# Optimization experiments

Measured on AMD Instinct MI355X. Metric: run time of the kernel, lower is better.

## Reference

```python
import jax, jax.numpy as jnp
from jax import lax
import numpy as np
import math

B = 2; H = 64; W = 64; HW = H * W
CIN = 128; CH = 64          # in_chans, in_chans//2
E = 192; DEPTH = 2          # embed_dim, depth
DIN = 384; DST = 4; DTR = 12; KC = 4   # d_inner, d_state, dt_rank, d_conv
NC = 9
SAMPLE = HW // 2            # round(h*w*self_ratio), self_ratio=0.5
LE = HW - SAMPLE            # number of mask==0 (easy) tokens per row


def setup_inputs() -> dict:
    key = jax.random.key(0)
    ks = jax.random.split(key, 16)
    rn = lambda k, s, sc: jax.random.normal(k, s, jnp.float32) * sc
    return {
        'x': rn(ks[0], (B, CIN, H, W), 1.0),
        'head_id': 0,
        'sp_w': rn(ks[1], (1, CH, 1, 1), 1.0 / math.sqrt(CH)),
        'sp_b': jnp.zeros((1,), jnp.float32),
        'c0_w': rn(ks[2], (E, CIN, 1, 1), 1.0 / math.sqrt(CIN)),
        'c0_b': jnp.zeros((E,), jnp.float32),
        'blk_norm_w': jnp.ones((DEPTH, E), jnp.float32),
        'blk_conv_w': rn(ks[3], (DEPTH, E, E, 3, 3), 1.0 / math.sqrt(9 * E)),
        'blk_conv_b': jnp.zeros((DEPTH, E), jnp.float32),
        'm_in_w': rn(ks[4], (DEPTH, 2 * DIN, E), 1.0 / math.sqrt(E)),
        'm_conv_w': rn(ks[5], (DEPTH, DIN, KC), 1.0 / math.sqrt(KC)),
        'm_conv_b': jnp.zeros((DEPTH, DIN), jnp.float32),
        'm_x_w': rn(ks[6], (DEPTH, DTR + 2 * DST, DIN), 1.0 / math.sqrt(DIN)),
        'm_dt_w': rn(ks[7], (DEPTH, DIN, DTR), 1.0 / math.sqrt(DTR)),
        'm_dt_b': rn(ks[8], (DEPTH, DIN), 0.1),
        'm_Alog': jnp.tile(jnp.log(jnp.arange(1, DST + 1, dtype=jnp.float32)), (DEPTH, DIN, 1)),
        'm_D': jnp.ones((DEPTH, DIN), jnp.float32),
        'm_out_w': rn(ks[9], (DEPTH, E, DIN), 1.0 / math.sqrt(DIN)),
        'ln_w': jnp.ones((E,), jnp.float32),
        'ln_b': jnp.zeros((E,), jnp.float32),
        'h_conv_w': rn(ks[10], (E, E, 3, 3), 1.0 / math.sqrt(9 * E)),
        'h_bn_w': jnp.ones((E,), jnp.float32),
        'h_bn_b': jnp.zeros((E,), jnp.float32),
        'h_cls_w': rn(ks[11], (NC, E, 1, 1), 1.0 / math.sqrt(E)),
        'h_cls_b': jnp.zeros((NC,), jnp.float32),
    }


def conv2d(x, w, b=None, pad=0, dil=1):
    y = lax.conv_general_dilated(x, w, (1, 1), [(pad, pad), (pad, pad)],
                                 rhs_dilation=(dil, dil),
                                 dimension_numbers=('NCHW', 'OIHW', 'NCHW'))
    return y if b is None else y + b[None, :, None, None]


def silu(x):
    return x * jax.nn.sigmoid(x)


def mamba_mixer(xe, in_w, conv_w, conv_b, x_w, dt_w, dt_b, Alog, Dp, out_w):
    # xe: [B, L, E] easy tokens; standard Mamba selective scan (d_state=4, d_conv=4)
    Bn, L, _ = xe.shape
    xz = jnp.einsum('ble,de->bld', xe, in_w)          # [B,L,2*DIN]
    xh, z = jnp.split(xz, 2, axis=-1)
    xp = jnp.pad(xh, ((0, 0), (KC - 1, 0), (0, 0)))   # causal depthwise conv
    xc = conv_b + sum(conv_w[:, k] * xp[:, k:k + L, :] for k in range(KC))
    xc = silu(xc)
    dbl = jnp.einsum('bld,rd->blr', xc, x_w)
    dt, Bm, Cm = dbl[..., :DTR], dbl[..., DTR:DTR + DST], dbl[..., DTR + DST:]
    dt = jax.nn.softplus(jnp.einsum('blr,dr->bld', dt, dt_w) + dt_b)
    A = -jnp.exp(Alog)                                 # [DIN, DST]
    dA = jnp.exp(dt[..., None] * A)                    # [B,L,DIN,DST]
    dBx = dt[..., None] * Bm[:, :, None, :] * xc[..., None]

    def step(h, inp):
        dA_t, dBx_t, C_t = inp
        h = dA_t * h + dBx_t
        return h, jnp.einsum('bdn,bn->bd', h, C_t)

    h0 = jnp.zeros((Bn, DIN, DST), xe.dtype)
    _, ys = lax.scan(step, h0, (jnp.moveaxis(dA, 1, 0), jnp.moveaxis(dBx, 1, 0), jnp.moveaxis(Cm, 1, 0)))
    y = jnp.moveaxis(ys, 0, 1) + Dp * xc
    y = y * silu(z)
    return jnp.einsum('bld,ed->ble', y, out_w)


def snm_forward(x, sp_w, sp_b, c0_w, c0_b, blk_norm_w, blk_conv_w, blk_conv_b,
                m_in_w, m_conv_w, m_conv_b, m_x_w, m_dt_w, m_dt_b, m_Alog, m_D, m_out_w,
                ln_w, ln_b, h_conv_w, h_bn_w, h_bn_b, h_cls_w, h_cls_b):
    res, imgf = jnp.split(x, 2, axis=1)
    res = res * res                                    # prepocess_residual('square')
    simple_pred = jax.nn.sigmoid(conv2d(res, sp_w, sp_b))
    scores = (simple_pred + res.mean(1, keepdims=True)).reshape(B, HW)
    idx = jnp.argsort(scores, axis=1)[:, :SAMPLE]      # topk smallest
    feats = imgf.transpose(0, 2, 3, 1).reshape(B, HW, CH)

    def per_batch(f_i, idx_i):
        bank = f_i[idx_i]                              # [SAMPLE, CH]
        d2 = (jnp.sum(f_i * f_i, -1, keepdims=True)
              + jnp.sum(bank * bank, -1)[None, :]
              - 2.0 * f_i @ bank.T)
        d = jnp.sqrt(jnp.maximum(d2, 0.0))
        d = d.at[idx_i, jnp.arange(SAMPLE)].set(jnp.inf)   # exclude self matches
        nns = jnp.argmin(lax.stop_gradient(d), axis=1)
        return bank[nns] - f_i

    sres = jax.vmap(per_batch)(feats, idx)
    sres = sres.reshape(B, H, W, CH).transpose(0, 3, 1, 2)
    sres = sres * sres                                 # prepocess_residual('square')
    x2 = jnp.concatenate([res, sres], axis=1)          # [B, CIN, H, W]

    mask = jnp.zeros((B, HW), jnp.float32).at[jnp.arange(B)[:, None], idx].set(1.0)
    easy_idx = jnp.argsort(mask, axis=1)[:, :LE]       # stable: mask==0 positions in order
    bidx = jnp.arange(B)[:, None]

    fea = conv2d(x2, c0_w, c0_b)                       # [B,E,H,W]
    hidden = fea.reshape(B, E, HW).transpose(0, 2, 1)  # [B,L,E]
    residual = None
    for d in range(DEPTH):
        residual = hidden if residual is None else hidden + residual
        hid = residual * lax.rsqrt(jnp.mean(residual * residual, -1, keepdims=True) + 1e-5) * blk_norm_w[d]
        him = hid.transpose(0, 2, 1).reshape(B, E, H, W)
        him = conv2d(him, blk_conv_w[d], blk_conv_b[d], pad=1)
        hid = him.reshape(B, E, HW).transpose(0, 2, 1)
        easy = hid[bidx, easy_idx]                     # gather mask==0 tokens
        mixed = mamba_mixer(easy, m_in_w[d], m_conv_w[d], m_conv_b[d], m_x_w[d],
                            m_dt_w[d], m_dt_b[d], m_Alog[d], m_D[d], m_out_w[d])
        hidden = hid.at[bidx, easy_idx].set(mixed)     # scatter back

    out = hidden + residual
    mu = out.mean(-1, keepdims=True)
    var = jnp.mean((out - mu) ** 2, -1, keepdims=True)
    out = (out - mu) * lax.rsqrt(var + 1e-5) * ln_w + ln_b
    f = out.transpose(0, 2, 1).reshape(B, E, H, W)

    # head (atrous_rate=3): dilated conv (no bias) + BN(eval, running stats 0/1) + ReLU + 1x1
    h1 = conv2d(f, h_conv_w, pad=3, dil=3)
    bn_scale = h_bn_w / jnp.sqrt(1.0 + 1e-5)
    h1 = jax.nn.relu(h1 * bn_scale[None, :, None, None] + h_bn_b[None, :, None, None])
    logits = conv2d(h1, h_cls_w, h_cls_b)
    return simple_pred, logits


def reference(x, head_id, sp_w, sp_b, c0_w, c0_b, blk_norm_w, blk_conv_w, blk_conv_b,
              m_in_w, m_conv_w, m_conv_b, m_x_w, m_dt_w, m_dt_b, m_Alog, m_D, m_out_w,
              ln_w, ln_b, h_conv_w, h_bn_w, h_bn_b, h_cls_w, h_cls_b):
    # head_id=0 selects branch 0; only branch-0 params are materialized.
    return snm_forward(x, sp_w, sp_b, c0_w, c0_b, blk_norm_w, blk_conv_w, blk_conv_b,
                       m_in_w, m_conv_w, m_conv_b, m_x_w, m_dt_w, m_dt_b, m_Alog, m_D, m_out_w,
                       ln_w, ln_b, h_conv_w, h_bn_w, h_bn_b, h_cls_w, h_cls_b)
```

## Files before the change

### kernel.cpp

```cpp
#include <hip/hip_runtime.h>
#include <hip/hip_bf16.h>
#include <math.h>

#define BB 2
#define HWp 4096
#define CH 64
#define CIN 128
#define EE 192
#define DIN 384
#define DST 4
#define DTR 12
#define KC 4
#define NCc 9
#define SAMPLE 2048
#define LEc 2048
#define NCH 128
#define CLEN 16
#define NSPLIT 8
#define PADW 70
#define PADP 3

typedef __attribute__((ext_vector_type(8))) short bf16x8;
typedef __attribute__((ext_vector_type(4))) float f32x4;

__device__ __forceinline__ float sigmoid_fast(float x){ return 1.0f/(1.0f+__expf(-x)); }
__device__ __forceinline__ float softplus_f(float x){ return fmaxf(x,0.0f) + log1pf(expf(-fabsf(x))); }

__device__ __forceinline__ void split_bf16(float v, unsigned short& h, unsigned short& l){
  __hip_bfloat16 bh = __float2bfloat16(v);
  h = *(unsigned short*)&bh;
  float r = v - __bfloat162float(bh);
  __hip_bfloat16 bl = __float2bfloat16(r);
  l = *(unsigned short*)&bl;
}

#define SZ_WTBLK_BF (2*9*EE*EE)
#define SZ_WTHEAD_BF (9*EE*EE)
#define SZ_WTIN (2*EE*2*DIN)
#define SZ_WTOUT (2*DIN*EE)
#define SZ_WTC0 (CIN*EE)
#define SZ_WT_TOTAL (SZ_WTBLK_BF+SZ_WTHEAD_BF+SZ_WTIN+SZ_WTOUT+SZ_WTC0)

__global__ void prep_weights(const float* blk_w, const float* head_w, const float* in_w,
                             const float* out_w, const float* c0_w,
                             __hip_bfloat16* wtb_blk, __hip_bfloat16* wtb_head,
                             float* wt_in, float* wt_out, float* wt_c0){
  int i = blockIdx.x*256 + threadIdx.x;
  if (i >= SZ_WT_TOTAL) return;
  int o = i;
  if (o < SZ_WTBLK_BF){
    int j = o & 7;
    int lane = (o>>3) & 63;
    int nt = (o/512) % 3;
    int e = (o/1536) % 6;
    int tap = (o/9216) % 9;
    int eoB = (o/82944) % 4;
    int d = o / 331776;
    int m = lane & 15, kg = lane >> 4;
    int eo = eoB*48 + nt*16 + m;
    int ei = e*32 + kg*8 + j;
    wtb_blk[o] = __float2bfloat16(blk_w[(((d*EE+eo)*EE+ei)*9)+tap]);
    return;
  }
  o -= SZ_WTBLK_BF;
  if (o < SZ_WTHEAD_BF){
    int j = o & 7;
    int lane = (o>>3) & 63;
    int nt = (o/512) % 3;
    int e = (o/1536) % 6;
    int tap = (o/9216) % 9;
    int eoB = (o/82944) % 4;
    int m = lane & 15, kg = lane >> 4;
    int eo = eoB*48 + nt*16 + m;
    int ei = e*32 + kg*8 + j;
    wtb_head[o] = __float2bfloat16(head_w[((eo*EE+ei)*9)+tap]);
    return;
  }
  o -= SZ_WTHEAD_BF;
  if (o < SZ_WTIN){
    int dd = o % (2*DIN); int e = (o/(2*DIN))%EE; int d = o/(2*DIN*EE);
    wt_in[o] = in_w[((d*2*DIN)+dd)*EE + e]; return;
  }
  o -= SZ_WTIN;
  if (o < SZ_WTOUT){
    int eo = o%EE; int dch=(o/EE)%DIN; int d = o/(EE*DIN);
    wt_out[o] = out_w[((d*EE+eo)*DIN)+dch]; return;
  }
  o -= SZ_WTOUT;
  { int e = o%EE; int c = o/EE;  wt_c0[o] = c0_w[e*CIN + c]; }
}

__global__ __launch_bounds__(256) void k_prep2(const float* __restrict__ x, const float* sp_w,
                       const float* sp_b, float* __restrict__ res2, float* __restrict__ feats,
                       float* scores, float* outSP){
  __shared__ float tile[CIN][33];
  int t = threadIdx.x;
  int p0 = blockIdx.x * 32;
  int b = p0 >> 12; int prow = p0 & 4095;
  const float* xb = x + (size_t)b*CIN*HWp + prow;
  #pragma unroll
  for (int i=0;i<4;i++){
    int idx = i*256 + t;
    int c = idx >> 3;
    int p4 = idx & 7;
    float4 v = *(const float4*)(xb + (size_t)c*HWp + p4*4);
    tile[c][p4*4+0]=v.x; tile[c][p4*4+1]=v.y; tile[c][p4*4+2]=v.z; tile[c][p4*4+3]=v.w;
  }
  __syncthreads();
  int lane = t & 63;
  int wv = t >> 6;
  float sw = sp_w[lane];
  float sb = sp_b[0];
  #pragma unroll
  for (int k=0;k<8;k++){
    int p = wv*8 + k;
    float v = tile[lane][p];
    float r2 = v*v;
    float f = tile[64+lane][p];
    int g = p0 + p;
    res2[(size_t)g*CH + lane] = r2;
    feats[(size_t)g*CH + lane] = f;
    float aS = r2*sw, aM = r2;
    #pragma unroll
    for (int msk=32; msk>0; msk>>=1){
      aS += __shfl_xor(aS, msk, 64);
      aM += __shfl_xor(aM, msk, 64);
    }
    if (lane == 0){
      float sp = 1.0f/(1.0f+expf(-(aS + sb)));
      outSP[g] = sp;
      scores[g] = sp + aM*(1.0f/CH);
    }
  }
}

__global__ void k_zero(int* p, int n){
  int g = blockIdx.x*256+threadIdx.x;
  if (g < n) p[g] = 0;
}

__global__ void k_rank2(const float* scores, int* ranks){
  int b = blockIdx.z;
  int t = threadIdx.x;
  int p = blockIdx.x*256 + t;
  int j0 = blockIdx.y*256;
  __shared__ float s[256];
  s[t] = scores[b*HWp + j0 + t];
  float sp = scores[b*HWp + p];
  __syncthreads();
  int r = 0;
  #pragma unroll 8
  for (int jj=0;jj<256;jj++){
    float sj = s[jj];
    int j = j0 + jj;
    r += (sj < sp || (sj == sp && j < p)) ? 1 : 0;
  }
  atomicAdd(&ranks[b*HWp+p], r);
}

__global__ __launch_bounds__(1024) void k_easy(const int* ranks, int* idx_sorted, int* easy_idx){
  int b = blockIdx.x; int t = threadIdx.x;
  __shared__ int buf[1024];
  int i0 = t*4;
  int r0 = ranks[b*HWp+i0];
  int r1 = ranks[b*HWp+i0+1];
  int r2 = ranks[b*HWp+i0+2];
  int r3 = ranks[b*HWp+i0+3];
  int f0 = r0 >= SAMPLE, f1 = r1 >= SAMPLE, f2 = r2 >= SAMPLE, f3 = r3 >= SAMPLE;
  if (!f0) idx_sorted[b*SAMPLE + r0] = i0;
  if (!f1) idx_sorted[b*SAMPLE + r1] = i0+1;
  if (!f2) idx_sorted[b*SAMPLE + r2] = i0+2;
  if (!f3) idx_sorted[b*SAMPLE + r3] = i0+3;
  int cnt = f0+f1+f2+f3;
  buf[t] = cnt;
  __syncthreads();
  for (int off=1; off<1024; off<<=1){
    int v = buf[t];
    int a = (t>=off) ? buf[t-off] : 0;
    __syncthreads();
    buf[t] = v + a;
    __syncthreads();
  }
  int pre = buf[t] - cnt;
  int base = b*LEc;
  if (f0) easy_idx[base+pre++] = i0;
  if (f1) easy_idx[base+pre++] = i0+1;
  if (f2) easy_idx[base+pre++] = i0+2;
  if (f3) easy_idx[base+pre]   = i0+3;
}

__global__ void k_split(const float* __restrict__ feats, unsigned short* __restrict__ fhi,
                        unsigned short* __restrict__ flo){
  int g = blockIdx.x*256 + threadIdx.x;
  float4 v = ((const float4*)feats)[g];
  ushort4 h, l;
  split_bf16(v.x, h.x, l.x);
  split_bf16(v.y, h.y, l.y);
  split_bf16(v.z, h.z, l.z);
  split_bf16(v.w, h.w, l.w);
  ((ushort4*)fhi)[g] = h;
  ((ushort4*)flo)[g] = l;
}

__global__ __launch_bounds__(64) void k_bank(const float* __restrict__ feats, const int* __restrict__ idx_sorted,
                       float* __restrict__ bnorm, unsigned short* __restrict__ bankhi,
                       unsigned short* __restrict__ banklo){
  int t = blockIdx.x*64+threadIdx.x;
  int b = t>>11;
  int row = idx_sorted[t];
  const float4* fr = (const float4*)(feats + (size_t)(b*HWp + row)*CH);
  ushort4* oh = (ushort4*)(bankhi + (size_t)t*CH);
  ushort4* ol = (ushort4*)(banklo + (size_t)t*CH);
  float s=0;
  #pragma unroll
  for (int k=0;k<16;k++){
    float4 v = fr[k];
    s += v.x*v.x+v.y*v.y+v.z*v.z+v.w*v.w;
    ushort4 h, l;
    split_bf16(v.x, h.x, l.x);
    split_bf16(v.y, h.y, l.y);
    split_bf16(v.z, h.z, l.z);
    split_bf16(v.w, h.w, l.w);
    oh[k] = h; ol[k] = l;
  }
  bnorm[t] = s;
}

__global__ __launch_bounds__(256) void k_nn_mfma(const unsigned short* __restrict__ fhi,
        const unsigned short* __restrict__ flo, const unsigned short* __restrict__ bankhi,
        const unsigned short* __restrict__ banklo, const float* __restrict__ bnorm,
        const int* __restrict__ idx_sorted, float* __restrict__ pval, int* __restrict__ pidx){
  int lane = threadIdx.x & 63;
  int wv = threadIdx.x >> 6;
  int m = lane & 15, kg = lane >> 4;
  int b = blockIdx.z;
  int qrel0 = blockIdx.x*64 + wv*16;
  int jsplit = blockIdx.y;
  const short* qh = (const short*)fhi + ((size_t)(b*HWp + qrel0 + m))*CH + kg*8;
  const short* ql = (const short*)flo + ((size_t)(b*HWp + qrel0 + m))*CH + kg*8;
  bf16x8 Ah0 = *(const bf16x8*)(qh);
  bf16x8 Ah1 = *(const bf16x8*)(qh + 32);
  bf16x8 Al0 = *(const bf16x8*)(ql);
  bf16x8 Al1 = *(const bf16x8*)(ql + 32);
  float best0=1e30f,best1=1e30f,best2=1e30f,best3=1e30f;
  int bj0=0,bj1=0,bj2=0,bj3=0;
  for (int jt=0; jt<16; jt++){
    int jb = jsplit*256 + jt*16;
    int j = jb + m;
    const short* bh = (const short*)bankhi + ((size_t)(b*SAMPLE + j))*CH + kg*8;
    const short* bl = (const short*)banklo + ((size_t)(b*SAMPLE + j))*CH + kg*8;
    bf16x8 Bh0 = *(const bf16x8*)(bh);
    bf16x8 Bh1 = *(const bf16x8*)(bh + 32);
    bf16x8 Bl0 = *(const bf16x8*)(bl);
    bf16x8 Bl1 = *(const bf16x8*)(bl + 32);
    f32x4 acc = {0,0,0,0};
    acc = __builtin_amdgcn_mfma_f32_16x16x32_bf16(Ah0, Bh0, acc, 0,0,0);
    acc = __builtin_amdgcn_mfma_f32_16x16x32_bf16(Ah1, Bh1, acc, 0,0,0);
    acc = __builtin_amdgcn_mfma_f32_16x16x32_bf16(Al0, Bh0, acc, 0,0,0);
    acc = __builtin_amdgcn_mfma_f32_16x16x32_bf16(Al1, Bh1, acc, 0,0,0);
    acc = __builtin_amdgcn_mfma_f32_16x16x32_bf16(Ah0, Bl0, acc, 0,0,0);
    acc = __builtin_amdgcn_mfma_f32_16x16x32_bf16(Ah1, Bl1, acc, 0,0,0);
    acc = __builtin_amdgcn_mfma_f32_16x16x32_bf16(Al0, Bl0, acc, 0,0,0);
    acc = __builtin_amdgcn_mfma_f32_16x16x32_bf16(Al1, Bl1, acc, 0,0,0);
    float bn = bnorm[b*SAMPLE + j];
    int src = idx_sorted[b*SAMPLE + j];
    float v0 = bn - 2.0f*acc[0];
    float v1 = bn - 2.0f*acc[1];
    float v2 = bn - 2.0f*acc[2];
    float v3 = bn - 2.0f*acc[3];
    int qp = qrel0 + kg*4;
    if (src != qp   && v0 < best0){ best0 = v0; bj0 = j; }
    if (src != qp+1 && v1 < best1){ best1 = v1; bj1 = j; }
    if (src != qp+2 && v2 < best2){ best2 = v2; bj2 = j; }
    if (src != qp+3 && v3 < best3){ best3 = v3; bj3 = j; }
  }
  #pragma unroll
  for (int mask=1; mask<16; mask<<=1){
    float ov; int oj;
    ov = __shfl_xor(best0, mask, 64); oj = __shfl_xor(bj0, mask, 64);
    if (ov < best0 || (ov == best0 && oj < bj0)){ best0 = ov; bj0 = oj; }
    ov = __shfl_xor(best1, mask, 64); oj = __shfl_xor(bj1, mask, 64);
    if (ov < best1 || (ov == best1 && oj < bj1)){ best1 = ov; bj1 = oj; }
    ov = __shfl_xor(best2, mask, 64); oj = __shfl_xor(bj2, mask, 64);
    if (ov < best2 || (ov == best2 && oj < bj2)){ best2 = ov; bj2 = oj; }
    ov = __shfl_xor(best3, mask, 64); oj = __shfl_xor(bj3, mask, 64);
    if (ov < best3 || (ov == best3 && oj < bj3)){ best3 = ov; bj3 = oj; }
  }
  if (m == 0){
    int qg = b*HWp + qrel0 + kg*4;
    pval[(qg+0)*NSPLIT + jsplit] = best0; pidx[(qg+0)*NSPLIT + jsplit] = bj0;
    pval[(qg+1)*NSPLIT + jsplit] = best1; pidx[(qg+1)*NSPLIT + jsplit] = bj1;
    pval[(qg+2)*NSPLIT + jsplit] = best2; pidx[(qg+2)*NSPLIT + jsplit] = bj2;
    pval[(qg+3)*NSPLIT + jsplit] = best3; pidx[(qg+3)*NSPLIT + jsplit] = bj3;
  }
}

__global__ __launch_bounds__(64) void k_nn_resolve(const float* feats, const int* idx_sorted,
                             const float* pval, const int* pidx, float* sres2){
  int q = blockIdx.x*64+threadIdx.x;
  int b = q>>12;
  float best = 1e30f; int bj = 0;
  for (int s=0;s<NSPLIT;s++){
    float v = pval[q*NSPLIT+s]; int j = pidx[q*NSPLIT+s];
    if (v < best){ best = v; bj = j; }
  }
  int row = idx_sorted[b*SAMPLE + bj];
  const float4* fr = (const float4*)(feats + (size_t)q*CH);
  const float4* br = (const float4*)(feats + (size_t)(b*HWp+row)*CH);
  float4* out = (float4*)(sres2 + (size_t)q*CH);
  #pragma unroll
  for (int k=0;k<16;k++){
    float4 a = br[k], c = fr[k];
    float4 r;
    r.x=a.x-c.x; r.y=a.y-c.y; r.z=a.z-c.z; r.w=a.w-c.w;
    r.x*=r.x; r.y*=r.y; r.z*=r.z; r.w*=r.w;
    out[k] = r;
  }
}

__global__ __launch_bounds__(192) void k_c0(const float* res2, const float* sres2, const float* wt_c0,
                                            const float* c0_b, float* hidden){
  __shared__ float xin[CIN][20];
  int base = blockIdx.x * 16;
  int t = threadIdx.x;
  for (int i=t; i<16*CIN; i+=192){
    int px = i >> 7, c = i & 127;
    float v = (c < CH) ? res2[(base+px)*CH + c] : sres2[(base+px)*CH + (c-CH)];
    xin[c][px] = v;
  }
  __syncthreads();
  int e = t;
  float bias = c0_b[e];
  float acc[16];
  #pragma unroll
  for (int px=0;px<16;px++) acc[px]=bias;
  for (int c=0;c<CIN;c++){
    float w = wt_c0[c*EE + e];
    const float4* vr = (const float4*)(&xin[c][0]);
    float4 v0=vr[0], v1=vr[1], v2=vr[2], v3=vr[3];
    acc[0]+=v0.x*w; acc[1]+=v0.y*w; acc[2]+=v0.z*w; acc[3]+=v0.w*w;
    acc[4]+=v1.x*w; acc[5]+=v1.y*w; acc[6]+=v1.z*w; acc[7]+=v1.w*w;
    acc[8]+=v2.x*w; acc[9]+=v2.y*w; acc[10]+=v2.z*w; acc[11]+=v2.w*w;
    acc[12]+=v3.x*w; acc[13]+=v3.y*w; acc[14]+=v3.z*w; acc[15]+=v3.w*w;
  }
  #pragma unroll
  for (int px=0;px<16;px++) hidden[(base+px)*EE + e] = acc[px];
}

__global__ __launch_bounds__(192) void k_rms(const float* hidden, float* residual,
                                             __hip_bfloat16* __restrict__ xpad,
                                             const float* norm_w, int first){
  int row = blockIdx.x; int e = threadIdx.x;
  int o = row*EE + e;
  float h = hidden[o];
  float r = first ? h : (h + residual[o]);
  residual[o] = r;
  float s = r*r;
  #pragma unroll
  for (int m=32;m>0;m>>=1) s += __shfl_xor(s, m, 64);
  __shared__ float red[3];
  if ((e&63)==0) red[e>>6] = s;
  __syncthreads();
  float tot = red[0]+red[1]+red[2];
  float rms = rsqrtf(tot*(1.0f/EE) + 1e-5f);
  int b = row >> 12; int p = row & 4095; int y = p >> 6; int x = p & 63;
  xpad[((size_t)(b*PADW + y + PADP)*PADW + (x + PADP))*EE + e] = __float2bfloat16(r*rms*norm_w[e]);
}

template<int DIL, int FUSE>
__global__ __launch_bounds__(256,3) void k_conv3s(const __hip_bfloat16* __restrict__ xp,
        const __hip_bfloat16* __restrict__ wt, const float* __restrict__ bias,
        const float* __restrict__ bnw, const float* __restrict__ bnb,
        float* __restrict__ out){
  __shared__ short wlds[2][9216];
  int t = threadIdx.x;
  int lane = t & 63;
  int wv = t >> 6;
  int m = lane & 15, kg = lane >> 4;
  int rb = blockIdx.x;
  int b = rb >> 6, y = rb & 63;
  int eoB = blockIdx.y;
  int x = wv*16 + m;
  const short* xs = (const short*)xp;
  const short* ws = (const short*)wt + (size_t)eoB * 82944;
  int aBase0 = ((b*PADW + y + PADP)*PADW + (x + PADP))*EE + kg*8;

  f32x4 acc0={0,0,0,0}, acc1={0,0,0,0}, acc2={0,0,0,0};

  {
    const ushort4* src = (const ushort4*)(ws);
    ushort4* dst = (ushort4*)(&wlds[0][0]);
    #pragma unroll
    for (int k=0;k<9;k++) dst[k*256+t] = src[k*256+t];
  }
  bf16x8 curA[6];
  {
    int aB = aBase0 + ((-1)*DIL*PADW + (-1)*DIL)*EE;
    #pragma unroll
    for (int e=0;e<6;e++) curA[e] = *(const bf16x8*)(xs + aB + e*32);
  }
  __syncthreads();

  for (int tap=0; tap<9; tap++){
    int cur = tap & 1;
    ushort4 nxtW[9];
    bf16x8 nxtA[6];
    if (tap < 8){
      const ushort4* src = (const ushort4*)(ws + (size_t)(tap+1)*9216);
      #pragma unroll
      for (int k=0;k<9;k++) nxtW[k] = src[k*256+t];
      int ky = (tap+1)/3, kx = (tap+1)%3;
      int aB = aBase0 + ((ky-1)*DIL*PADW + (kx-1)*DIL)*EE;
      #pragma unroll
      for (int e=0;e<6;e++) nxtA[e] = *(const bf16x8*)(xs + aB + e*32);
    }
    const short* bl = &wlds[cur][0];
    #pragma unroll
    for (int e=0;e<6;e++){
      bf16x8 b0 = *(const bf16x8*)(bl + (e*3+0)*512 + lane*8);
      bf16x8 b1 = *(const bf16x8*)(bl + (e*3+1)*512 + lane*8);
      bf16x8 b2 = *(const bf16x8*)(bl + (e*3+2)*512 + lane*8);
      acc0 = __builtin_amdgcn_mfma_f32_16x16x32_bf16(curA[e], b0, acc0, 0,0,0);
      acc1 = __builtin_amdgcn_mfma_f32_16x16x32_bf16(curA[e], b1, acc1, 0,0,0);
      acc2 = __builtin_amdgcn_mfma_f32_16x16x32_bf16(curA[e], b2, acc2, 0,0,0);
    }
    if (tap < 8){
      ushort4* dst = (ushort4*)(&wlds[cur^1][0]);
      #pragma unroll
      for (int k=0;k<9;k++) dst[k*256+t] = nxtW[k];
      #pragma unroll
      for (int e=0;e<6;e++) curA[e] = nxtA[e];
    }
    __syncthreads();
  }

  int px0 = y*64 + wv*16 + kg*4;
  #pragma unroll
  for (int nt=0; nt<3; nt++){
    f32x4 a = (nt==0)?acc0:((nt==1)?acc1:acc2);
    int eo = eoB*48 + nt*16 + m;
    float add=0.0f, scale=0.0f, sh=0.0f;
    if (FUSE){ scale = bnw[eo]*rsqrtf(1.0f+1e-5f); sh = bnb[eo]; }
    else add = bias[eo];
    #pragma unroll
    for (int r=0;r<4;r++){
      float v = a[r];
      if (FUSE) v = fmaxf(v*scale + sh, 0.0f);
      else v += add;
      out[((size_t)(b*HWp) + px0 + r)*EE + eo] = v;
    }
  }
}

__global__ __launch_bounds__(256) void k_inproj(const float* hid2, const int* easy_idx, const float* wt_in_d,
                                                float* xh, float* zb){
  __shared__ float sh[EE][12];
  int bid = blockIdx.x;
  int b = bid >> 8; int l0 = (bid & 255)*8;
  int t = threadIdx.x;
  for (int i=t; i<8*EE; i+=256){
    int l = i/EE; int e = i - l*EE;
    int row = easy_idx[b*LEc + l0 + l];
    sh[e][l] = hid2[(b*HWp + row)*EE + e];
  }
  __syncthreads();
  float acc0[8], acc1[8], acc2[8];
  #pragma unroll
  for (int l=0;l<8;l++){ acc0[l]=0; acc1[l]=0; acc2[l]=0; }
  for (int e=0;e<EE;e++){
    float w0 = wt_in_d[e*768 + t];
    float w1 = wt_in_d[e*768 + t + 256];
    float w2 = wt_in_d[e*768 + t + 512];
    const float4* vr = (const float4*)(&sh[e][0]);
    float4 a = vr[0], c = vr[1];
    float v[8] = {a.x,a.y,a.z,a.w,c.x,c.y,c.z,c.w};
    #pragma unroll
    for (int l=0;l<8;l++){ acc0[l]+=v[l]*w0; acc1[l]+=v[l]*w1; acc2[l]+=v[l]*w2; }
  }
  #pragma unroll
  for (int k=0;k<3;k++){
    int dd = t + k*256;
    #pragma unroll
    for (int l=0;l<8;l++){
      float o = (k==0)?acc0[l]:((k==1)?acc1[l]:acc2[l]);
      int rb = b*LEc + l0 + l;
      if (dd < DIN) xh[rb*DIN + dd] = o;
      else zb[rb*DIN + dd - DIN] = o;
    }
  }
}

__global__ __launch_bounds__(128) void k_mpre(const float* xh, const float* cw, const float* cb,
                                              const float* xw, const float* dtw, const float* dtb_w,
                                              float* xc, float* bc, float* dtb){
  int row = blockIdx.x;
  int l = row & 2047;
  int t = threadIdx.x;
  __shared__ float sxc[DIN];
  __shared__ float sdbl[20];
  for (int i=t; i<DIN; i+=128){
    const float* w = cw + i*KC;
    float s = cb[i];
    #pragma unroll
    for (int k=0;k<KC;k++){
      int ls = l - 3 + k;
      if (ls >= 0) s += w[k]*xh[(row-3+k)*DIN + i];
    }
    s = s * sigmoid_fast(s);
    sxc[i] = s;
    xc[row*DIN+i] = s;
  }
  __syncthreads();
  if (t < 20){
    const float* w = xw + t*DIN;
    float a=0,b2=0,c=0,d2=0;
    for (int i=0;i<DIN;i+=4){ a+=sxc[i]*w[i]; b2+=sxc[i+1]*w[i+1]; c+=sxc[i+2]*w[i+2]; d2+=sxc[i+3]*w[i+3]; }
    float o = a+b2+c+d2;
    sdbl[t] = o;
    if (t >= DTR) bc[row*8 + (t-DTR)] = o;
  }
  __syncthreads();
  for (int i=t; i<DIN; i+=128){
    const float* w = dtw + i*DTR;
    float s = dtb_w[i];
    #pragma unroll
    for (int k=0;k<DTR;k++) s += sdbl[k]*w[k];
    dtb[row*DIN+i] = softplus_f(s);
  }
}

__global__ void k_scanA(const float* dt, const float* xc, const float* bc, const float* Alog, float* chnk){
  int g = blockIdx.x*256+threadIdx.x;
  int dch = g % DIN; int c = (g/DIN) % NCH; int b = g/(DIN*NCH);
  float A[4], P[4]={1,1,1,1}, h[4]={0,0,0,0};
  #pragma unroll
  for (int n=0;n<4;n++) A[n] = -__expf(Alog[dch*DST+n]);
  int lbase = b*LEc + c*CLEN;
  for (int s=0;s<CLEN;s++){
    int base = lbase + s;
    float dtv = dt[base*DIN + dch];
    float xcv = xc[base*DIN + dch];
    float dx = dtv*xcv;
    #pragma unroll
    for (int n=0;n<4;n++){
      float dA = __expf(dtv*A[n]);
      float Bn = bc[base*8 + n];
      h[n] = dA*h[n] + dx*Bn;
      P[n] *= dA;
    }
  }
  float* o = chnk + (size_t)g*8;
  #pragma unroll
  for (int n=0;n<4;n++){ o[n]=P[n]; o[4+n]=h[n]; }
}

__global__ void k_scanB(const float* chnk, float* hin){
  int g = blockIdx.x*256+threadIdx.x;
  if (g >= BB*DIN) return;
  int dch = g % DIN; int b = g / DIN;
  float h0=0,h1=0,h2=0,h3=0;
  for (int cb=0; cb<NCH/8; cb++){
    float4 P[8], Hl[8];
    #pragma unroll
    for (int u=0;u<8;u++){
      const float4* cp = (const float4*)(chnk + (size_t)((b*NCH + cb*8+u)*DIN + dch)*8);
      P[u] = cp[0]; Hl[u] = cp[1];
    }
    #pragma unroll
    for (int u=0;u<8;u++){
      int idx = (b*NCH + cb*8+u)*DIN + dch;
      float4 hv; hv.x=h0; hv.y=h1; hv.z=h2; hv.w=h3;
      *(float4*)(hin + (size_t)idx*4) = hv;
      h0 = P[u].x*h0 + Hl[u].x;
      h1 = P[u].y*h1 + Hl[u].y;
      h2 = P[u].z*h2 + Hl[u].z;
      h3 = P[u].w*h3 + Hl[u].w;
    }
  }
}

__global__ void k_scanC(const float* dt, const float* xc, const float* zb, const float* bc, const float* Alog,
                        const float* Dw, const float* hin, float* yb){
  int g = blockIdx.x*256+threadIdx.x;
  int dch = g % DIN; int c = (g/DIN) % NCH; int b = g/(DIN*NCH);
  float A[4], h[4];
  #pragma unroll
  for (int n=0;n<4;n++){ A[n] = -__expf(Alog[dch*DST+n]); h[n] = hin[(size_t)g*4+n]; }
  float Dv = Dw[dch];
  int lbase = b*LEc + c*CLEN;
  for (int s=0;s<CLEN;s++){
    int base = lbase + s;
    float dtv = dt[base*DIN+dch];
    float xcv = xc[base*DIN+dch];
    float zv  = zb[base*DIN+dch];
    float dx = dtv*xcv;
    float y = 0.0f;
    #pragma unroll
    for (int n=0;n<4;n++){
      float dA = __expf(dtv*A[n]);
      h[n] = dA*h[n] + dx*bc[base*8+n];
      y += h[n]*bc[base*8+4+n];
    }
    y = (y + Dv*xcv) * (zv * sigmoid_fast(zv));
    yb[base*DIN + dch] = y;
  }
}

__global__ __launch_bounds__(192) void k_outproj(const float* yb, const int* easy_idx, const float* wt_out_d,
                                                 float* hidden){
  __shared__ float sy[DIN][20];
  int bid = blockIdx.x; int b = bid >> 7; int l0 = (bid & 127)*16;
  int t = threadIdx.x;
  for (int i=t; i<16*DIN; i+=192){
    int l = i/DIN; int c = i - l*DIN;
    sy[c][l] = yb[(b*LEc + l0 + l)*DIN + c];
  }
  __syncthreads();
  float acc[16];
  #pragma unroll
  for (int l=0;l<16;l++) acc[l]=0;
  for (int c=0;c<DIN;c++){
    float w = wt_out_d[c*EE + t];
    const float4* vr = (const float4*)(&sy[c][0]);
    float4 a=vr[0], b4=vr[1], c4=vr[2], d4=vr[3];
    acc[0]+=a.x*w;  acc[1]+=a.y*w;  acc[2]+=a.z*w;  acc[3]+=a.w*w;
    acc[4]+=b4.x*w; acc[5]+=b4.y*w; acc[6]+=b4.z*w; acc[7]+=b4.w*w;
    acc[8]+=c4.x*w; acc[9]+=c4.y*w; acc[10]+=c4.z*w; acc[11]+=c4.w*w;
    acc[12]+=d4.x*w; acc[13]+=d4.y*w; acc[14]+=d4.z*w; acc[15]+=d4.w*w;
  }
  #pragma unroll
  for (int l=0;l<16;l++){
    int row = easy_idx[b*LEc + l0 + l];
    hidden[(b*HWp + row)*EE + t] = acc[l];
  }
}

__global__ __launch_bounds__(192) void k_ln(const float* hidden, const float* residual,
                                            const float* lnw, const float* lnb,
                                            __hip_bfloat16* __restrict__ xpad){
  int row = blockIdx.x; int e = threadIdx.x;
  int o = row*EE + e;
  float v = hidden[o] + residual[o];
  __shared__ float redA[3], redB[3];
  float s = v;
  #pragma unroll
  for (int m=32;m>0;m>>=1) s += __shfl_xor(s, m, 64);
  if ((e&63)==0) redA[e>>6] = s;
  __syncthreads();
  float mu = (redA[0]+redA[1]+redA[2])*(1.0f/EE);
  float dv = v - mu;
  float s2 = dv*dv;
  #pragma unroll
  for (int m=32;m>0;m>>=1) s2 += __shfl_xor(s2, m, 64);
  if ((e&63)==0) redB[e>>6] = s2;
  __syncthreads();
  float var = (redB[0]+redB[1]+redB[2])*(1.0f/EE);
  float o2 = dv*rsqrtf(var + 1e-5f)*lnw[e] + lnb[e];
  int b = row >> 12; int p = row & 4095; int y = p >> 6; int x = p & 63;
  xpad[((size_t)(b*PADW + y + PADP)*PADW + (x + PADP))*EE + e] = __float2bfloat16(o2);
}

__global__ __launch_bounds__(64) void k_cls(const float* h1, const float* cls_w, const float* cls_b, float* out){
  __shared__ float wsm[NCc][EE];
  int t = threadIdx.x;
  for (int i=t; i<NCc*EE; i+=64){ wsm[i/EE][i%EE] = cls_w[i]; }
  __syncthreads();
  int g = blockIdx.x*64 + t;
  int p = g & 4095; int b = g >> 12;
  const float4* hrow = (const float4*)(h1 + (size_t)g*EE);
  float acc[NCc];
  #pragma unroll
  for (int n=0;n<NCc;n++) acc[n] = cls_b[n];
  for (int c4=0;c4<EE/4;c4++){
    float4 h = hrow[c4];
    #pragma unroll
    for (int n=0;n<NCc;n++){
      const float4 wv = *(const float4*)(&wsm[n][c4*4]);
      acc[n] += h.x*wv.x + h.y*wv.y + h.z*wv.z + h.w*wv.w;
    }
  }
  #pragma unroll
  for (int n=0;n<NCc;n++)
    out[((size_t)b*NCc + n)*HWp + p] = acc[n];
}

extern "C" void kernel_launch(void* const* d_in, const int* in_sizes, int n_in,
                              void* d_out, int out_size, void* d_ws, size_t ws_size,
                              hipStream_t stream) {
  const float* x          = (const float*)d_in[0];
  const float* sp_w       = (const float*)d_in[2];
  const float* sp_b       = (const float*)d_in[3];
  const float* c0_w       = (const float*)d_in[4];
  const float* c0_b       = (const float*)d_in[5];
  const float* blk_norm_w = (const float*)d_in[6];
  const float* blk_conv_w = (const float*)d_in[7];
  const float* blk_conv_b = (const float*)d_in[8];
  const float* m_in_w     = (const float*)d_in[9];
  const float* m_conv_w   = (const float*)d_in[10];
  const float* m_conv_b   = (const float*)d_in[11];
  const float* m_x_w      = (const float*)d_in[12];
  const float* m_dt_w     = (const float*)d_in[13];
  const float* m_dt_b     = (const float*)d_in[14];
  const float* m_Alog     = (const float*)d_in[15];
  const float* m_D        = (const float*)d_in[16];
  const float* m_out_w    = (const float*)d_in[17];
  const float* ln_w       = (const float*)d_in[18];
  const float* ln_b       = (const float*)d_in[19];
  const float* h_conv_w   = (const float*)d_in[20];
  const float* h_bn_w     = (const float*)d_in[21];
  const float* h_bn_b     = (const float*)d_in[22];
  const float* h_cls_w    = (const float*)d_in[23];
  const float* h_cls_b    = (const float*)d_in[24];

  float* out_sp     = (float*)d_out;
  float* out_logits = (float*)d_out + BB*HWp;

  float* w = (float*)d_ws;
  size_t off = 0;
  auto alloc = [&](size_t n){ float* p = w + off; off += (n + 63) & ~size_t(63); return p; };
  float* res2    = alloc(BB*HWp*CH);
  float* sres2   = alloc(BB*HWp*CH);
  float* feats   = alloc(BB*HWp*CH);
  float* scores  = alloc(BB*HWp);
  float* bnorm   = alloc(BB*SAMPLE);
  float* hidden  = alloc(BB*HWp*EE);
  float* residual= alloc(BB*HWp*EE);
  float* hid2    = alloc(BB*HWp*EE);
  float* xh      = alloc(BB*LEc*DIN);
  float* zb      = alloc(BB*LEc*DIN);
  float* xc      = alloc(BB*LEc*DIN);
  float* dtb     = alloc(BB*LEc*DIN);
  float* yb      = alloc(BB*LEc*DIN);
  float* bcbuf   = alloc(BB*LEc*8);
  float* pval    = alloc(BB*HWp*NSPLIT);
  float* chnk    = alloc((size_t)BB*NCH*DIN*8);
  float* hin     = alloc((size_t)BB*NCH*DIN*4);
  float* wt_in   = alloc(SZ_WTIN);
  float* wt_out  = alloc(SZ_WTOUT);
  float* wt_c0   = alloc(SZ_WTC0);
  __hip_bfloat16* wtb_blk  = (__hip_bfloat16*)alloc(SZ_WTBLK_BF/2);
  __hip_bfloat16* wtb_head = (__hip_bfloat16*)alloc(SZ_WTHEAD_BF/2);
  __hip_bfloat16* xpad     = (__hip_bfloat16*)alloc(BB*PADW*PADW*EE/2);
  unsigned short* fhi    = (unsigned short*)alloc(BB*HWp*CH/2);
  unsigned short* flo    = (unsigned short*)alloc(BB*HWp*CH/2);
  unsigned short* bankhi = (unsigned short*)alloc(BB*SAMPLE*CH/2);
  unsigned short* banklo = (unsigned short*)alloc(BB*SAMPLE*CH/2);
  int* pidx       = (int*)alloc(BB*HWp*NSPLIT);
  int* idx_sorted = (int*)alloc(BB*SAMPLE);
  int* ranks      = (int*)alloc(BB*HWp);
  int* easy_idx   = (int*)alloc(BB*LEc);
  if (off*sizeof(float) > ws_size) return;

  prep_weights<<<(SZ_WT_TOTAL+255)/256, 256, 0, stream>>>(blk_conv_w, h_conv_w, m_in_w, m_out_w, c0_w,
                                                          wtb_blk, wtb_head, wt_in, wt_out, wt_c0);
  k_zero<<<(BB*PADW*PADW*EE/2+255)/256, 256, 0, stream>>>((int*)xpad, BB*PADW*PADW*EE/2);
  k_prep2<<<BB*HWp/32, 256, 0, stream>>>(x, sp_w, sp_b, res2, feats, scores, out_sp);
  k_zero<<<(BB*HWp+255)/256, 256, 0, stream>>>(ranks, BB*HWp);
  k_rank2<<<dim3(16,16,BB), 256, 0, stream>>>(scores, ranks);
  k_split<<<BB*HWp*CH/4/256, 256, 0, stream>>>(feats, fhi, flo);
  k_easy<<<BB, 1024, 0, stream>>>(ranks, idx_sorted, easy_idx);
  k_bank<<<BB*SAMPLE/64, 64, 0, stream>>>(feats, idx_sorted, bnorm, bankhi, banklo);
  k_nn_mfma<<<dim3(HWp/64, NSPLIT, BB), 256, 0, stream>>>(fhi, flo, bankhi, banklo, bnorm,
                                                          idx_sorted, pval, pidx);
  k_nn_resolve<<<BB*HWp/64, 64, 0, stream>>>(feats, idx_sorted, pval, pidx, sres2);
  k_c0<<<BB*HWp/16, 192, 0, stream>>>(res2, sres2, wt_c0, c0_b, hidden);

  for (int d=0; d<2; d++){
    k_rms<<<BB*HWp, 192, 0, stream>>>(hidden, residual, xpad, blk_norm_w + d*EE, d==0);
    k_conv3s<1,0><<<dim3(BB*64,4), 256, 0, stream>>>(xpad, wtb_blk + d*9*EE*EE,
                                                     blk_conv_b + d*EE, nullptr, nullptr, hidden);
    k_inproj<<<BB*(LEc/8), 256, 0, stream>>>(hidden, easy_idx, wt_in + d*EE*2*DIN, xh, zb);
    k_mpre<<<BB*LEc, 128, 0, stream>>>(xh, m_conv_w + d*DIN*KC, m_conv_b + d*DIN,
                                       m_x_w + d*(DTR+2*DST)*DIN, m_dt_w + d*DIN*DTR, m_dt_b + d*DIN,
                                       xc, bcbuf, dtb);
    k_scanA<<<BB*NCH*DIN/256, 256, 0, stream>>>(dtb, xc, bcbuf, m_Alog + d*DIN*DST, chnk);
    k_scanB<<<(BB*DIN+255)/256, 256, 0, stream>>>(chnk, hin);
    k_scanC<<<BB*NCH*DIN/256, 256, 0, stream>>>(dtb, xc, zb, bcbuf, m_Alog + d*DIN*DST,
                                                m_D + d*DIN, hin, yb);
    k_outproj<<<BB*(LEc/16), 192, 0, stream>>>(yb, easy_idx, wt_out + d*DIN*EE, hidden);
  }

  k_ln<<<BB*HWp, 192, 0, stream>>>(hidden, residual, ln_w, ln_b, xpad);
  k_conv3s<3,1><<<dim3(BB*64,4), 256, 0, stream>>>(xpad, wtb_head, nullptr, h_bn_w, h_bn_b, hid2);
  k_cls<<<BB*HWp/64, 64, 0, stream>>>(hid2, h_cls_w, h_cls_b, out_logits);
}
```

Before: 435.2 us.

## Fuse prep kernels: zeroing into weight prep, split into prep2, bank into easy, resolve into c0

```diff
diff --git a/kernel.cpp b/kernel.cpp
--- a/kernel.cpp
+++ b/kernel.cpp
@@ -40,13 +40,16 @@
 #define SZ_WTOUT (2*DIN*EE)
 #define SZ_WTC0 (CIN*EE)
 #define SZ_WT_TOTAL (SZ_WTBLK_BF+SZ_WTHEAD_BF+SZ_WTIN+SZ_WTOUT+SZ_WTC0)
+#define NXPI (BB*PADW*PADW*EE/2)
+#define NRANKS (BB*HWp)
 
 __global__ void prep_weights(const float* blk_w, const float* head_w, const float* in_w,
                              const float* out_w, const float* c0_w,
                              __hip_bfloat16* wtb_blk, __hip_bfloat16* wtb_head,
-                             float* wt_in, float* wt_out, float* wt_c0){
+                             float* wt_in, float* wt_out, float* wt_c0,
+                             int* xpad_i, int* ranks){
   int i = blockIdx.x*256 + threadIdx.x;
-  if (i >= SZ_WT_TOTAL) return;
+  if (i >= SZ_WT_TOTAL + NXPI + NRANKS) return;
   int o = i;
   if (o < SZ_WTBLK_BF){
     int j = o & 7;
@@ -87,11 +90,18 @@
     wt_out[o] = out_w[((d*EE+eo)*DIN)+dch]; return;
   }
   o -= SZ_WTOUT;
-  { int e = o%EE; int c = o/EE;  wt_c0[o] = c0_w[e*CIN + c]; }
+  if (o < SZ_WTC0){
+    int e = o%EE; int c = o/EE;  wt_c0[o] = c0_w[e*CIN + c]; return;
+  }
+  o -= SZ_WTC0;
+  if (o < NXPI){ xpad_i[o] = 0; return; }
+  o -= NXPI;
+  ranks[o] = 0;
 }
 
 __global__ __launch_bounds__(256) void k_prep2(const float* __restrict__ x, const float* sp_w,
                        const float* sp_b, float* __restrict__ res2, float* __restrict__ feats,
+                       unsigned short* __restrict__ fhi, unsigned short* __restrict__ flo,
                        float* scores, float* outSP){
   __shared__ float tile[CIN][33];
   int t = threadIdx.x;
@@ -120,6 +130,10 @@
     int g = p0 + p;
     res2[(size_t)g*CH + lane] = r2;
     feats[(size_t)g*CH + lane] = f;
+    unsigned short hh, ll;
+    split_bf16(f, hh, ll);
+    fhi[(size_t)g*CH + lane] = hh;
+    flo[(size_t)g*CH + lane] = ll;
     float aS = r2*sw, aM = r2;
     #pragma unroll
     for (int msk=32; msk>0; msk>>=1){
@@ -132,11 +146,6 @@
       scores[g] = sp + aM*(1.0f/CH);
     }
   }
-}
-
-__global__ void k_zero(int* p, int n){
-  int g = blockIdx.x*256+threadIdx.x;
-  if (g < n) p[g] = 0;
 }
 
 __global__ void k_rank2(const float* scores, int* ranks){
@@ -158,7 +167,10 @@
   atomicAdd(&ranks[b*HWp+p], r);
 }
 
-__global__ __launch_bounds__(1024) void k_easy(const int* ranks, int* idx_sorted, int* easy_idx){
+__global__ __launch_bounds__(1024) void k_easy(const int* ranks, int* idx_sorted, int* easy_idx,
+                                               const float* __restrict__ feats, float* __restrict__ bnorm,
+                                               unsigned short* __restrict__ bankhi,
+                                               unsigned short* __restrict__ banklo){
   int b = blockIdx.x; int t = threadIdx.x;
   __shared__ int buf[1024];
   int i0 = t*4;
@@ -187,43 +199,26 @@
   if (f1) easy_idx[base+pre++] = i0+1;
   if (f2) easy_idx[base+pre++] = i0+2;
   if (f3) easy_idx[base+pre]   = i0+3;
-}
-
-__global__ void k_split(const float* __restrict__ feats, unsigned short* __restrict__ fhi,
-                        unsigned short* __restrict__ flo){
-  int g = blockIdx.x*256 + threadIdx.x;
-  float4 v = ((const float4*)feats)[g];
-  ushort4 h, l;
-  split_bf16(v.x, h.x, l.x);
-  split_bf16(v.y, h.y, l.y);
-  split_bf16(v.z, h.z, l.z);
-  split_bf16(v.w, h.w, l.w);
-  ((ushort4*)fhi)[g] = h;
-  ((ushort4*)flo)[g] = l;
-}
-
-__global__ __launch_bounds__(64) void k_bank(const float* __restrict__ feats, const int* __restrict__ idx_sorted,
-                       float* __restrict__ bnorm, unsigned short* __restrict__ bankhi,
-                       unsigned short* __restrict__ banklo){
-  int t = blockIdx.x*64+threadIdx.x;
-  int b = t>>11;
-  int row = idx_sorted[t];
-  const float4* fr = (const float4*)(feats + (size_t)(b*HWp + row)*CH);
-  ushort4* oh = (ushort4*)(bankhi + (size_t)t*CH);
-  ushort4* ol = (ushort4*)(banklo + (size_t)t*CH);
-  float s=0;
-  #pragma unroll
-  for (int k=0;k<16;k++){
-    float4 v = fr[k];
-    s += v.x*v.x+v.y*v.y+v.z*v.z+v.w*v.w;
-    ushort4 h, l;
-    split_bf16(v.x, h.x, l.x);
-    split_bf16(v.y, h.y, l.y);
-    split_bf16(v.z, h.z, l.z);
-    split_bf16(v.w, h.w, l.w);
-    oh[k] = h; ol[k] = l;
-  }
-  bnorm[t] = s;
+  __syncthreads();
+  for (int r = t; r < SAMPLE; r += 1024){
+    int row = idx_sorted[b*SAMPLE + r];
+    const float4* fr = (const float4*)(feats + (size_t)(b*HWp + row)*CH);
+    ushort4* oh = (ushort4*)(bankhi + (size_t)(b*SAMPLE + r)*CH);
+    ushort4* ol = (ushort4*)(banklo + (size_t)(b*SAMPLE + r)*CH);
+    float s=0;
+    #pragma unroll
+    for (int k=0;k<16;k++){
+      float4 v = fr[k];
+      s += v.x*v.x+v.y*v.y+v.z*v.z+v.w*v.w;
+      ushort4 h, l;
+      split_bf16(v.x, h.x, l.x);
+      split_bf16(v.y, h.y, l.y);
+      split_bf16(v.z, h.z, l.z);
+      split_bf16(v.w, h.w, l.w);
+      oh[k] = h; ol[k] = l;
+    }
+    bnorm[b*SAMPLE + r] = s;
+  }
 }
 
 __global__ __launch_bounds__(256) void k_nn_mfma(const unsigned short* __restrict__ fhi,
@@ -295,37 +290,35 @@
   }
 }
 
-__global__ __launch_bounds__(64) void k_nn_resolve(const float* feats, const int* idx_sorted,
-                             const float* pval, const int* pidx, float* sres2){
-  int q = blockIdx.x*64+threadIdx.x;
-  int b = q>>12;
-  float best = 1e30f; int bj = 0;
-  for (int s=0;s<NSPLIT;s++){
-    float v = pval[q*NSPLIT+s]; int j = pidx[q*NSPLIT+s];
-    if (v < best){ best = v; bj = j; }
-  }
-  int row = idx_sorted[b*SAMPLE + bj];
-  const float4* fr = (const float4*)(feats + (size_t)q*CH);
-  const float4* br = (const float4*)(feats + (size_t)(b*HWp+row)*CH);
-  float4* out = (float4*)(sres2 + (size_t)q*CH);
-  #pragma unroll
-  for (int k=0;k<16;k++){
-    float4 a = br[k], c = fr[k];
-    float4 r;
-    r.x=a.x-c.x; r.y=a.y-c.y; r.z=a.z-c.z; r.w=a.w-c.w;
-    r.x*=r.x; r.y*=r.y; r.z*=r.z; r.w*=r.w;
-    out[k] = r;
-  }
-}
-
-__global__ __launch_bounds__(192) void k_c0(const float* res2, const float* sres2, const float* wt_c0,
-                                            const float* c0_b, float* hidden){
+__global__ __launch_bounds__(192) void k_c0(const float* res2, const float* __restrict__ feats,
+                                            const int* idx_sorted, const float* pval, const int* pidx,
+                                            const float* wt_c0, const float* c0_b, float* hidden){
   __shared__ float xin[CIN][20];
+  __shared__ int brow[16];
   int base = blockIdx.x * 16;
+  int b = base >> 12;
   int t = threadIdx.x;
+  if (t < 16){
+    int q = base + t;
+    float best = 1e30f; int bj = 0;
+    #pragma unroll
+    for (int s=0;s<NSPLIT;s++){
+      float v = pval[q*NSPLIT+s]; int j = pidx[q*NSPLIT+s];
+      if (v < best){ best = v; bj = j; }
+    }
+    brow[t] = idx_sorted[b*SAMPLE + bj];
+  }
+  __syncthreads();
   for (int i=t; i<16*CIN; i+=192){
     int px = i >> 7, c = i & 127;
-    float v = (c < CH) ? res2[(base+px)*CH + c] : sres2[(base+px)*CH + (c-CH)];
+    float v;
+    if (c < CH) v = res2[(size_t)(base+px)*CH + c];
+    else {
+      int cc = c - CH;
+      float a = feats[(size_t)(b*HWp + brow[px])*CH + cc];
+      float f = feats[(size_t)(base+px)*CH + cc];
+      float d = a - f; v = d*d;
+    }
     xin[c][px] = v;
   }
   __syncthreads();
@@ -344,7 +337,7 @@
     acc[12]+=v3.x*w; acc[13]+=v3.y*w; acc[14]+=v3.z*w; acc[15]+=v3.w*w;
   }
   #pragma unroll
-  for (int px=0;px<16;px++) hidden[(base+px)*EE + e] = acc[px];
+  for (int px=0;px<16;px++) hidden[(size_t)(base+px)*EE + e] = acc[px];
 }
 
 __global__ __launch_bounds__(192) void k_rms(const float* hidden, float* residual,
@@ -454,34 +447,34 @@
 
 __global__ __launch_bounds__(256) void k_inproj(const float* hid2, const int* easy_idx, const float* wt_in_d,
                                                 float* xh, float* zb){
-  __shared__ float sh[EE][12];
+  __shared__ float sh[EE][17];
   int bid = blockIdx.x;
-  int b = bid >> 8; int l0 = (bid & 255)*8;
+  int b = bid >> 7; int l0 = (bid & 127)*16;
   int t = threadIdx.x;
-  for (int i=t; i<8*EE; i+=256){
+  for (int i=t; i<16*EE; i+=256){
     int l = i/EE; int e = i - l*EE;
     int row = easy_idx[b*LEc + l0 + l];
-    sh[e][l] = hid2[(b*HWp + row)*EE + e];
-  }
-  __syncthreads();
-  float acc0[8], acc1[8], acc2[8];
-  #pragma unroll
-  for (int l=0;l<8;l++){ acc0[l]=0; acc1[l]=0; acc2[l]=0; }
+    sh[e][l] = hid2[(size_t)(b*HWp + row)*EE + e];
+  }
+  __syncthreads();
+  float acc0[16], acc1[16], acc2[16];
+  #pragma unroll
+  for (int l=0;l<16;l++){ acc0[l]=0; acc1[l]=0; acc2[l]=0; }
   for (int e=0;e<EE;e++){
     float w0 = wt_in_d[e*768 + t];
     float w1 = wt_in_d[e*768 + t + 256];
     float w2 = wt_in_d[e*768 + t + 512];
     const float4* vr = (const float4*)(&sh[e][0]);
-    float4 a = vr[0], c = vr[1];
-    float v[8] = {a.x,a.y,a.z,a.w,c.x,c.y,c.z,c.w};
-    #pragma unroll
-    for (int l=0;l<8;l++){ acc0[l]+=v[l]*w0; acc1[l]+=v[l]*w1; acc2[l]+=v[l]*w2; }
+    float4 a = vr[0], c = vr[1], d = vr[2], q = vr[3];
+    float v[16] = {a.x,a.y,a.z,a.w,c.x,c.y,c.z,c.w,d.x,d.y,d.z,d.w,q.x,q.y,q.z,q.w};
+    #pragma unroll
+    for (int l=0;l<16;l++){ acc0[l]+=v[l]*w0; acc1[l]+=v[l]*w1; acc2[l]+=v[l]*w2; }
   }
   #pragma unroll
   for (int k=0;k<3;k++){
     int dd = t + k*256;
     #pragma unroll
-    for (int l=0;l<8;l++){
+    for (int l=0;l<16;l++){
       float o = (k==0)?acc0[l]:((k==1)?acc1[l]:acc2[l]);
       int rb = b*LEc + l0 + l;
       if (dd < DIN) xh[rb*DIN + dd] = o;
@@ -631,7 +624,7 @@
   #pragma unroll
   for (int l=0;l<16;l++){
     int row = easy_idx[b*LEc + l0 + l];
-    hidden[(b*HWp + row)*EE + t] = acc[l];
+    hidden[(size_t)(b*HWp + row)*EE + t] = acc[l];
   }
 }
 
@@ -719,7 +712,6 @@
   size_t off = 0;
   auto alloc = [&](size_t n){ float* p = w + off; off += (n + 63) & ~size_t(63); return p; };
   float* res2    = alloc(BB*HWp*CH);
-  float* sres2   = alloc(BB*HWp*CH);
   float* feats   = alloc(BB*HWp*CH);
   float* scores  = alloc(BB*HWp);
   float* bnorm   = alloc(BB*SAMPLE);
@@ -751,25 +743,21 @@
   int* easy_idx   = (int*)alloc(BB*LEc);
   if (off*sizeof(float) > ws_size) return;
 
-  prep_weights<<<(SZ_WT_TOTAL+255)/256, 256, 0, stream>>>(blk_conv_w, h_conv_w, m_in_w, m_out_w, c0_w,
-                                                          wtb_blk, wtb_head, wt_in, wt_out, wt_c0);
-  k_zero<<<(BB*PADW*PADW*EE/2+255)/256, 256, 0, stream>>>((int*)xpad, BB*PADW*PADW*EE/2);
-  k_prep2<<<BB*HWp/32, 256, 0, stream>>>(x, sp_w, sp_b, res2, feats, scores, out_sp);
-  k_zero<<<(BB*HWp+255)/256, 256, 0, stream>>>(ranks, BB*HWp);
+  prep_weights<<<(SZ_WT_TOTAL+NXPI+NRANKS+255)/256, 256, 0, stream>>>(
+      blk_conv_w, h_conv_w, m_in_w, m_out_w, c0_w,
+      wtb_blk, wtb_head, wt_in, wt_out, wt_c0, (int*)xpad, ranks);
+  k_prep2<<<BB*HWp/32, 256, 0, stream>>>(x, sp_w, sp_b, res2, feats, fhi, flo, scores, out_sp);
   k_rank2<<<dim3(16,16,BB), 256, 0, stream>>>(scores, ranks);
-  k_split<<<BB*HWp*CH/4/256, 256, 0, stream>>>(feats, fhi, flo);
-  k_easy<<<BB, 1024, 0, stream>>>(ranks, idx_sorted, easy_idx);
-  k_bank<<<BB*SAMPLE/64, 64, 0, stream>>>(feats, idx_sorted, bnorm, bankhi, banklo);
+  k_easy<<<BB, 1024, 0, stream>>>(ranks, idx_sorted, easy_idx, feats, bnorm, bankhi, banklo);
   k_nn_mfma<<<dim3(HWp/64, NSPLIT, BB), 256, 0, stream>>>(fhi, flo, bankhi, banklo, bnorm,
                                                           idx_sorted, pval, pidx);
-  k_nn_resolve<<<BB*HWp/64, 64, 0, stream>>>(feats, idx_sorted, pval, pidx, sres2);
-  k_c0<<<BB*HWp/16, 192, 0, stream>>>(res2, sres2, wt_c0, c0_b, hidden);
+  k_c0<<<BB*HWp/16, 192, 0, stream>>>(res2, feats, idx_sorted, pval, pidx, wt_c0, c0_b, hidden);
 
   for (int d=0; d<2; d++){
     k_rms<<<BB*HWp, 192, 0, stream>>>(hidden, residual, xpad, blk_norm_w + d*EE, d==0);
     k_conv3s<1,0><<<dim3(BB*64,4), 256, 0, stream>>>(xpad, wtb_blk + d*9*EE*EE,
                                                      blk_conv_b + d*EE, nullptr, nullptr, hidden);
-    k_inproj<<<BB*(LEc/8), 256, 0, stream>>>(hidden, easy_idx, wt_in + d*EE*2*DIN, xh, zb);
+    k_inproj<<<BB*(LEc/16), 256, 0, stream>>>(hidden, easy_idx, wt_in + d*EE*2*DIN, xh, zb);
     k_mpre<<<BB*LEc, 128, 0, stream>>>(xh, m_conv_w + d*DIN*KC, m_conv_b + d*DIN,
                                        m_x_w + d*(DTR+2*DST)*DIN, m_dt_w + d*DIN*DTR, m_dt_b + d*DIN,
                                        xc, bcbuf, dtb);
```

Result: slower. 559.1 us (+28.5%).
